# Optimization experiments

Hardware: AMD Instinct MI355X
Metric: run time of the kernel (lower is better)

Reference implementation:

```python
import jax, jax.numpy as jnp
import numpy as np

B, S, D_IN, D, K, KU, L, M, H = 2, 1024, 64, 512, 16, 3, 2, 2, 2048
N_FFT = 2048  # next power of two >= 2*S - 1 (preconvolve padded_sl)
EPS = 1e-5


def setup_inputs() -> dict:
    key = jax.random.key(0)
    ks = jax.random.split(key, 8)
    # Hankel matrix Z[i,j] = 2 / ((i+j)^3 - (i+j)), i,j in 1..S; top-K eigh
    i = np.arange(1, S + 1, dtype=np.float64)
    s = i[:, None] + i[None, :]
    Z = 2.0 / (s ** 3 - s)
    evals, evecs = np.linalg.eigh(Z)
    sigma = jnp.asarray(evals[-K:], jnp.float32)          # (K,)
    phi = jnp.asarray(evecs[:, -K:], jnp.float32)         # (S, K)
    std = D ** -0.5
    return dict(
        inputs=jax.random.normal(ks[0], (B, S, D_IN), jnp.float32),
        sigma=sigma,
        phi=phi,
        in_proj_w=jax.random.normal(ks[1], (M, D, D_IN), jnp.float32) * (D_IN ** -0.5),
        rn_w=jnp.ones((M, L, D), jnp.float32),
        M_u=jax.random.uniform(ks[2], (M, L, KU, D, D), jnp.float32, -std, std),
        M_phi_plus=jax.random.normal(ks[3], (M, L, K, D, D), jnp.float32) * std,
        M_phi_minus=jax.random.normal(ks[4], (M, L, K, D, D), jnp.float32) * std,
        fc1_w=jax.random.normal(ks[5], (M, L, 2 * H, D), jnp.float32) * std,
        fc2_w=jax.random.normal(ks[6], (M, L, D, H), jnp.float32) * (H ** -0.5),
        out_proj_w=jax.random.normal(ks[7], (M, D_IN, D), jnp.float32) * std,
    )


def rmsnorm(x, w):
    return x * jax.lax.rsqrt(jnp.mean(x * x, axis=-1, keepdims=True) + EPS) * w


def compute_spectral(x, sigma, phi, mp, mm):
    # x: (B,S,D); phi: (S,K); mp/mm: (K,D,D)
    sgn = jnp.where(jnp.arange(S) % 2 == 0, 1.0, -1.0).astype(x.dtype)
    u2 = jnp.stack([x, x * sgn[None, :, None]], axis=-1)            # (B,S,D,2)
    U = jnp.fft.rfft(u2, n=N_FFT, axis=1)                           # (B,nf,D,2)
    Vf = jnp.fft.rfft(phi, n=N_FFT, axis=0)                         # (nf,K)
    Uc = jnp.fft.irfft(Vf[None, :, :, None, None] * U[:, :, None, :, :], n=N_FFT, axis=1)[:, :S]  # (B,S,K,D,2)
    Up = Uc[..., 0]
    Um = Uc[..., 1] * sgn[None, :, None, None]
    sig4 = sigma ** 0.25
    return (jnp.einsum('bskd,k,kdo->bso', Up, sig4, mp)
            + jnp.einsum('bskd,k,kdo->bso', Um, sig4, mm))


def compute_ar_u(mu, x):
    # y_t = sum_i x_{t-i} @ M_u[i]; mu: (KU,D,D)
    out = jnp.einsum('bsd,do->bso', x, mu[0])
    for i in range(1, KU):
        xi = jnp.pad(x[:, :S - i], ((0, 0), (i, 0), (0, 0)))
        out = out + jnp.einsum('bsd,do->bso', xi, mu[i])
    return out


def gated_mlp(x, w1, w2):
    y = x @ w1.T
    y, gate = jnp.split(y, 2, axis=-1)
    return (y * jax.nn.silu(gate)) @ w2.T


def reference(inputs, sigma, phi, in_proj_w, rn_w, M_u, M_phi_plus, M_phi_minus, fc1_w, fc2_w, out_proj_w):
    preds = jnp.zeros((B, S, D_IN), inputs.dtype)
    for m in range(M):  # ResidualSTU: sum of per-model predictions
        x = inputs @ in_proj_w[m].T
        for l in range(L):
            z = x
            h = rmsnorm(x, rn_w[m, l])
            spec = compute_spectral(h, sigma, phi, M_phi_plus[m, l], M_phi_minus[m, l])
            y_t = spec + compute_ar_u(M_u[m, l], h)  # use_ar_u=True, use_ar_y=False
            x = x + y_t
            x = x + gated_mlp(x, fc1_w[m, l], fc2_w[m, l])
            x = x + z
        preds = preds + x @ out_proj_w[m].T
    return preds
```

## Files before the change

### kernel.cpp

```cpp
#include <hip/hip_runtime.h>
#include <hip/hip_bf16.h>

typedef _Float16 f16;
typedef _Float16 half8 __attribute__((ext_vector_type(8)));
typedef float f32x4 __attribute__((ext_vector_type(4)));

#define S_LEN 1024
#define DMODEL 512
#define NFFT   2048
#define RPB    2048
#define RTOT   4096
#define CPS    1064
#define NROW   2048
#define NPART  4

__device__ __forceinline__ float2 mkf2(float a, float b) { float2 r; r.x = a; r.y = b; return r; }
__device__ __forceinline__ int zp(int i) { return i + (i >> 5); }
__device__ __forceinline__ float2 cmul(float2 w, float2 b) {
  return mkf2(b.x * w.x - b.y * w.y, b.x * w.y + b.y * w.x);
}
__device__ __forceinline__ float2 f2a(float2 a, float2 b) { return mkf2(a.x + b.x, a.y + b.y); }
__device__ __forceinline__ float2 f2s(float2 a, float2 b) { return mkf2(a.x - b.x, a.y - b.y); }

__device__ __forceinline__ void gl16(const f16* g, f16* l) {
  __builtin_amdgcn_global_load_lds((const __attribute__((address_space(1))) void*)g,
                                   (__attribute__((address_space(3))) void*)l, 16, 0, 0);
}

template<bool INV>
__device__ __forceinline__ void fft2048(float2* z, const float2* __restrict__ tw, int tid) {
  for (int i = tid; i < 2048; i += 256) {
    int j = (int)(__brev((unsigned)i) >> 21);
    if (i < j) { float2 a = z[zp(i)]; z[zp(i)] = z[zp(j)]; z[zp(j)] = a; }
  }
  __syncthreads();
#pragma unroll
  for (int r8 = 0; r8 < 3; ++r8) {
    const int sl = 1 + 3 * r8;
    const int h = 1 << (sl - 1);
    {
      int q = tid;
      int j = q & (h - 1);
      int i0 = ((q >> (sl - 1)) << (sl + 2)) + j;
      float2 a0 = z[zp(i0)],         a1 = z[zp(i0 + h)];
      float2 a2 = z[zp(i0 + 2 * h)], a3 = z[zp(i0 + 3 * h)];
      float2 a4 = z[zp(i0 + 4 * h)], a5 = z[zp(i0 + 5 * h)];
      float2 a6 = z[zp(i0 + 6 * h)], a7 = z[zp(i0 + 7 * h)];
      float2 wA  = tw[j << (11 - sl)];
      float2 wB0 = tw[j << (10 - sl)];
      float2 wB1 = tw[(j + h) << (10 - sl)];
      float2 wC0 = tw[j << (9 - sl)];
      float2 wC1 = tw[(j + h) << (9 - sl)];
      float2 wC2 = tw[(j + 2 * h) << (9 - sl)];
      float2 wC3 = tw[(j + 3 * h) << (9 - sl)];
      if (INV) {
        wA.y = -wA.y; wB0.y = -wB0.y; wB1.y = -wB1.y;
        wC0.y = -wC0.y; wC1.y = -wC1.y; wC2.y = -wC2.y; wC3.y = -wC3.y;
      }
      float2 t;
      t = cmul(wA, a1); float2 b0 = f2a(a0, t), b1 = f2s(a0, t);
      t = cmul(wA, a3); float2 b2 = f2a(a2, t), b3 = f2s(a2, t);
      t = cmul(wA, a5); float2 b4 = f2a(a4, t), b5 = f2s(a4, t);
      t = cmul(wA, a7); float2 b6 = f2a(a6, t), b7 = f2s(a6, t);
      t = cmul(wB0, b2); float2 c0 = f2a(b0, t), c2 = f2s(b0, t);
      t = cmul(wB1, b3); float2 c1 = f2a(b1, t), c3 = f2s(b1, t);
      t = cmul(wB0, b6); float2 c4 = f2a(b4, t), c6 = f2s(b4, t);
      t = cmul(wB1, b7); float2 c5 = f2a(b5, t), c7 = f2s(b5, t);
      t = cmul(wC0, c4); z[zp(i0)]         = f2a(c0, t); z[zp(i0 + 4 * h)] = f2s(c0, t);
      t = cmul(wC1, c5); z[zp(i0 + h)]     = f2a(c1, t); z[zp(i0 + 5 * h)] = f2s(c1, t);
      t = cmul(wC2, c6); z[zp(i0 + 2 * h)] = f2a(c2, t); z[zp(i0 + 6 * h)] = f2s(c2, t);
      t = cmul(wC3, c7); z[zp(i0 + 3 * h)] = f2a(c3, t); z[zp(i0 + 7 * h)] = f2s(c3, t);
    }
    __syncthreads();
  }
  for (int q = tid; q < 512; q += 256) {
    float2 a0 = z[zp(q)], a1 = z[zp(q + 512)], a2 = z[zp(q + 1024)], a3 = z[zp(q + 1536)];
    float2 w1 = tw[q << 1], w2 = tw[q], w3 = tw[q + 512];
    if (INV) { w1.y = -w1.y; w2.y = -w2.y; w3.y = -w3.y; }
    float2 t;
    t = cmul(w1, a1); float2 b0 = f2a(a0, t), b1 = f2s(a0, t);
    t = cmul(w1, a3); float2 b2 = f2a(a2, t), b3 = f2s(a2, t);
    t = cmul(w2, b2); z[zp(q)]        = f2a(b0, t); z[zp(q + 1024)] = f2s(b0, t);
    t = cmul(w3, b3); z[zp(q + 512)]  = f2a(b1, t); z[zp(q + 1536)] = f2s(b1, t);
  }
  __syncthreads();
}

__global__ void k_twiddle(float2* tw) {
  int i = blockIdx.x * 256 + threadIdx.x;
  if (i < 1024) {
    float ang = -6.2831853071795864769f * (float)i / 2048.0f;
    tw[i] = mkf2(cosf(ang), sinf(ang));
  }
}

__global__ void k_fft_phi(const float* __restrict__ phi, float2* __restrict__ Vf,
                          const float2* __restrict__ tw) {
  __shared__ float2 z[2112];
  int tid = threadIdx.x;
  int k0 = blockIdx.x * 2;
  for (int t = tid; t < 1024; t += 256)
    z[zp(t)] = *(const float2*)(phi + (size_t)t * 16 + k0);
  for (int t = 1024 + tid; t < 2048; t += 256) z[zp(t)] = mkf2(0.f, 0.f);
  __syncthreads();
  fft2048<false>(z, tw, tid);
  for (int f = tid; f <= 1024; f += 256) {
    float2 zf = z[zp(f)], zc = z[zp((2048 - f) & 2047)];
    Vf[(size_t)k0 * 1025 + f]       = mkf2(0.5f * (zf.x + zc.x), 0.5f * (zf.y - zc.y));
    Vf[(size_t)(k0 + 1) * 1025 + f] = mkf2(0.5f * (zf.y + zc.y), 0.5f * (zc.x - zf.x));
  }
}

__global__ void k_cpcm(const float2* __restrict__ Vf, const float* __restrict__ sigma,
                       float2* __restrict__ cpcm) {
  int idx = blockIdx.x * 256 + threadIdx.x;
  if (idx >= 32 * CPS) return;
  int kb = idx / CPS, f = idx - kb * CPS;
  int k = kb & 15;
  float s = powf(sigma[k], 0.25f) * (1.0f / 2048.0f);
  float2 v = mkf2(0.f, 0.f);
  if (f == 0) {
    float dc = Vf[(size_t)k * 1025].x;
    float ny = Vf[(size_t)k * 1025 + 1024].x;
    v = (kb < 16) ? mkf2(s * dc, s * ny) : mkf2(s * ny, s * dc);
  } else if (f <= 1023) {
    if (kb < 16) {
      v = Vf[(size_t)k * 1025 + f];
    } else {
      float2 t = Vf[(size_t)k * 1025 + (1024 - f)];
      v = mkf2(t.x, -t.y);
    }
    v.x *= s; v.y *= s;
  }
  cpcm[idx] = v;
}

__global__ __launch_bounds__(256)
void k_fwdcast(const f16* __restrict__ hb2, f16* __restrict__ Xbf,
               const float2* __restrict__ tw, int li,
               const float* __restrict__ Mp, const float* __restrict__ Mm,
               const float* __restrict__ Mu, const float* __restrict__ Fc1,
               const float* __restrict__ Fc2,
               f16* __restrict__ Wsp, f16* __restrict__ Wu,
               f16* __restrict__ Wf1, f16* __restrict__ Wf2) {
  __shared__ __align__(16) char smem[16896];
  int wg = (int)blockIdx.x, tid = threadIdx.x;
  if (wg < 1024) {
    float2* z = (float2*)smem;
    int model = wg >> 9;
    int b = (wg >> 8) & 1;
    int d0 = (wg & 255) * 2;
    const f16* hsrc = hb2 + (size_t)(model * 2 + b) * 1026 * 512;
    f16* xdst = Xbf + (size_t)model * RTOT * 512 + (size_t)b * RPB * 512;
    for (int t = tid; t < 1024; t += 256) {
      union { unsigned v; f16 q[2]; } w;
      w.v = *(const unsigned*)(hsrc + (size_t)(2 + t) * 512 + d0);
      z[zp(t)] = mkf2((float)w.q[0], (float)w.q[1]);
    }
    for (int t = 1024 + tid; t < 2048; t += 256) z[zp(t)] = mkf2(0.f, 0.f);
    __syncthreads();
    fft2048<false>(z, tw, tid);
    for (int f = tid; f <= 1024; f += 256) {
      float2 zf = z[zp(f)], zc = z[zp((2048 - f) & 2047)];
      float x0r = 0.5f * (zf.x + zc.x), x0i = 0.5f * (zf.y - zc.y);
      float x1r = 0.5f * (zf.y + zc.y), x1i = 0.5f * (zc.x - zf.x);
      union { f16 h2[2]; unsigned u; } pr, pi;
      pr.h2[0] = (f16)x0r; pr.h2[1] = (f16)x1r;
      pi.h2[0] = (f16)x0i; pi.h2[1] = (f16)x1i;
      if (f == 0) {
        *(unsigned*)(xdst + d0) = pr.u;
      } else if (f == 1024) {
        *(unsigned*)(xdst + (size_t)512 + d0) = pr.u;
      } else {
        *(unsigned*)(xdst + (size_t)(2 * f) * 512 + d0)     = pr.u;
        *(unsigned*)(xdst + (size_t)(2 * f + 1) * 512 + d0) = pi.u;
      }
    }
    return;
  }
  float* T = (float*)smem;
  int q0all = wg - 1024;
  int model = q0all & 1;
  int blk = q0all >> 1;
  int ml = model * 2 + li;
  const float* mp  = Mp  + (size_t)ml * 16 * 262144;
  const float* mm  = Mm  + (size_t)ml * 16 * 262144;
  const float* mu  = Mu  + (size_t)ml * 3 * 262144;
  const float* fc1 = Fc1 + (size_t)ml * 4096 * 512;
  const float* fc2 = Fc2 + (size_t)ml * 512 * 2048;
  f16* WspM = Wsp + (size_t)model * 16384 * 512;
  f16* WuM  = Wu  + (size_t)model * 512 * 1536;
  f16* Wf1M = Wf1 + (size_t)model * 4096 * 512;
  f16* Wf2M = Wf2 + (size_t)model * 512 * 2048;
  if (blk < 2048) {
    int mat = blk >> 6, tile = blk & 63;
    int d0 = (tile >> 3) * 64, o0 = (tile & 7) * 64;
    const float* src = (mat < 16) ? (mp + (size_t)mat * 262144)
                                  : (mm + (size_t)(mat - 16) * 262144);
    for (int q = tid; q < 4096; q += 256) {
      int i = q >> 6, j = q & 63;
      T[i * 65 + j] = src[(size_t)(d0 + i) * 512 + o0 + j];
    }
    __syncthreads();
    for (int q = tid; q < 4096; q += 256) {
      int i = q >> 6, j = q & 63;
      WspM[(size_t)(mat * 512 + o0 + i) * 512 + d0 + j] = (f16)T[j * 65 + i];
    }
  } else if (blk < 2240) {
    int q1 = blk - 2048;
    int ip = q1 >> 6, tile = q1 & 63;
    int d0 = (tile >> 3) * 64, o0 = (tile & 7) * 64;
    const float* src = mu + (size_t)(2 - ip) * 262144;
    for (int q = tid; q < 4096; q += 256) {
      int i = q >> 6, j = q & 63;
      T[i * 65 + j] = src[(size_t)(d0 + i) * 512 + o0 + j];
    }
    __syncthreads();
    for (int q = tid; q < 4096; q += 256) {
      int i = q >> 6, j = q & 63;
      WuM[(size_t)(o0 + i) * 1536 + ip * 512 + d0 + j] = (f16)T[j * 65 + i];
    }
  } else if (blk < 3264) {
    int q1 = blk - 2240;
    size_t e = ((size_t)q1 * 256 + tid) * 8;
    int jj = (int)(e >> 9), col = (int)(e & 511);
    int srow = (jj & 1) ? (2048 + (jj >> 1)) : (jj >> 1);
    const float4* s = (const float4*)(fc1 + (size_t)srow * 512 + col);
    float4 a = s[0], b = s[1];
    union { f16 h[8]; uint4 u; } pk;
    pk.h[0] = (f16)a.x; pk.h[1] = (f16)a.y; pk.h[2] = (f16)a.z; pk.h[3] = (f16)a.w;
    pk.h[4] = (f16)b.x; pk.h[5] = (f16)b.y; pk.h[6] = (f16)b.z; pk.h[7] = (f16)b.w;
    *(uint4*)(Wf1M + (size_t)jj * 512 + col) = pk.u;
  } else {
    int q1 = blk - 3264;
    size_t e = ((size_t)q1 * 256 + tid) * 8;
    const float4* s = (const float4*)(fc2 + e);
    float4 a = s[0], b = s[1];
    union { f16 h[8]; uint4 u; } pk;
    pk.h[0] = (f16)a.x; pk.h[1] = (f16)a.y; pk.h[2] = (f16)a.z; pk.h[3] = (f16)a.w;
    pk.h[4] = (f16)b.x; pk.h[5] = (f16)b.y; pk.h[6] = (f16)b.z; pk.h[7] = (f16)b.w;
    *(uint4*)(Wf2M + e) = pk.u;
  }
}

__global__ void k_rmsnorm(const f16* __restrict__ x, const float* __restrict__ rn_w, int li,
                          f16* __restrict__ hb2) {
  int tid = threadIdx.x, l = tid & 63, wv = tid >> 6;
  int r = blockIdx.x * 4 + wv;
  int model = r >> 11;
  int rl = r & 2047;
  int b = rl >> 10, t = rl & 1023;
  const float* w = rn_w + (size_t)(model * 2 + li) * 512;
  const f16* xr = x + (size_t)r * 512;
  f16* hr = hb2 + (size_t)((model * 2 + b) * 1026 + 2 + t) * 512;
  float v[8]; float ss = 0.f;
#pragma unroll
  for (int j = 0; j < 8; ++j) { v[j] = (float)xr[j * 64 + l]; ss += v[j] * v[j]; }
#pragma unroll
  for (int o = 32; o; o >>= 1) ss += __shfl_xor(ss, o, 64);
  float rn = rsqrtf(ss * (1.f / 512.f) + 1e-5f);
#pragma unroll
  for (int j = 0; j < 8; ++j) {
    float hv = v[j] * rn * w[j * 64 + l];
    hr[j * 64 + l] = (f16)hv;
  }
}

__global__ void k_fft_inv(const f16* __restrict__ P, f16* __restrict__ spec,
                          const float2* __restrict__ tw) {
  __shared__ float2 z[2112];
  int tid = threadIdx.x;
  int wg = (int)blockIdx.x;
  int model = wg >> 9;
  int b = (wg >> 8) & 1;
  int o0 = (wg & 255) * 2;
  const f16* Pm = P + (size_t)model * 512 * RTOT;
  for (int fp = tid; fp < 512; fp += 256) {
    int f0 = fp * 2;
    size_t base0 = (size_t)o0 * RTOT + (size_t)b * RPB + 2 * f0;
    float s0r[2] = {0.f, 0.f}, s0i[2] = {0.f, 0.f};
    float s1r[2] = {0.f, 0.f}, s1i[2] = {0.f, 0.f};
#pragma unroll
    for (int g = 0; g < NPART; ++g) {
      const f16* Pg = Pm + (size_t)g * (2ull * 512 * RTOT);
      union { uint2 u; f16 h[4]; } ua, uc;
      ua.u = *(const uint2*)(Pg + base0);
      uc.u = *(const uint2*)(Pg + base0 + RTOT);
      s0r[0] += (float)ua.h[0]; s0i[0] += (float)ua.h[1];
      s0r[1] += (float)ua.h[2]; s0i[1] += (float)ua.h[3];
      s1r[0] += (float)uc.h[0]; s1i[0] += (float)uc.h[1];
      s1r[1] += (float)uc.h[2]; s1i[1] += (float)uc.h[3];
    }
    if (fp == 0) {
      z[zp(0)]    = mkf2(s0r[0], s1r[0]);
      z[zp(1024)] = mkf2(s0i[0], s1i[0]);
    } else {
      z[zp(f0)]        = mkf2(s0r[0] - s1i[0], s0i[0] + s1r[0]);
      z[zp(2048 - f0)] = mkf2(s0r[0] + s1i[0], s1r[0] - s0i[0]);
    }
    int f1 = f0 + 1;
    z[zp(f1)]        = mkf2(s0r[1] - s1i[1], s0i[1] + s1r[1]);
    z[zp(2048 - f1)] = mkf2(s0r[1] + s1i[1], s1r[1] - s0i[1]);
  }
  __syncthreads();
  fft2048<true>(z, tw, tid);
  f16* sdst = spec + (size_t)(model * 2048 + b * 1024) * 512;
  for (int t = tid; t < 1024; t += 256) {
    float2 v = z[zp(t)];
    union { f16 h[2]; unsigned u; } pk;
    pk.h[0] = (f16)v.x; pk.h[1] = (f16)v.y;
    *(unsigned*)(sdst + (size_t)t * 512 + o0) = pk.u;
  }
}

__global__ __launch_bounds__(256, 2)
void k_gemm0(const f16* __restrict__ A0, const f16* __restrict__ B00,
             const float* __restrict__ aux0, f16* __restrict__ outP) {
  __shared__ __align__(16) f16 As[128 * 64];
  __shared__ __align__(16) f16 Bs[128 * 64];
  const int tid = threadIdx.x, l = tid & 63, wvi = tid >> 6;
  const int wr = wvi >> 1, wc = wvi & 1;
  int wg = (int)blockIdx.x;
  wg = (wg & 7) * 128 + (wg >> 3);
  const int model = wg >> 9;
  int rem = wg & 511;
  const int bz = rem >> 7; rem &= 127;
  const int by = rem >> 2, bx = rem & 3;
  const int r0 = by * 128, c0 = bx * 128;
  const f16* A  = A0  + (size_t)model * RTOT * 512;
  const f16* B0 = B00 + (size_t)model * 16384 * 512;

  f32x4 acc[4][4];
  f32x4 crun[4][4];
  f32x4 zz = {0.f, 0.f, 0.f, 0.f};
#pragma unroll
  for (int m = 0; m < 4; ++m)
#pragma unroll
    for (int n = 0; n < 4; ++n) { acc[m][n] = zz; crun[m][n] = zz; }

  const int rowl = tid >> 3;
  const int lc8 = ((tid & 7) ^ (rowl & 7)) * 8;
  f16* lA = As + ((tid >> 6) << 9);
  f16* lB = Bs + ((tid >> 6) << 9);
  const int lr = l & 15, kg = l >> 4, sw = l & 7;

  for (int s = 0; s < 64; ++s) {
    __syncthreads();
    {
      const int kA = (s & 7) * 64;
      const int kb = bz * 8 + (s >> 3);
#pragma unroll
      for (int i = 0; i < 4; ++i) {
        gl16(A + (size_t)(r0 + i * 32 + rowl) * 512 + kA + lc8, lA + i * 2048);
        gl16(B0 + (size_t)(kb * 512 + c0 + i * 32 + rowl) * 512 + kA + lc8, lB + i * 2048);
      }
    }
    __syncthreads();
#pragma unroll
    for (int kk = 0; kk < 2; ++kk) {
      half8 af[4], bf[4];
      const int pc8 = (((kk * 4 + kg) ^ sw) << 3);
#pragma unroll
      for (int m = 0; m < 4; ++m)
        af[m] = *(const half8*)(As + (wr * 64 + m * 16 + lr) * 64 + pc8);
#pragma unroll
      for (int n = 0; n < 4; ++n)
        bf[n] = *(const half8*)(Bs + (wc * 64 + n * 16 + lr) * 64 + pc8);
#pragma unroll
      for (int m = 0; m < 4; ++m)
#pragma unroll
        for (int n = 0; n < 4; ++n)
          acc[m][n] = __builtin_amdgcn_mfma_f32_16x16x32_f16(af[m], bf[n], acc[m][n], 0, 0, 0);
    }
    if ((s & 7) == 7) {
      int kb = bz * 8 + (s >> 3);
#pragma unroll
      for (int m = 0; m < 4; ++m) {
        int R = r0 + wr * 64 + m * 16 + (kg << 2);
        int rb = R & (RPB - 1);
        bool dc = (rb == 0);
        float4 cs = *(const float4*)(aux0 + (size_t)kb * (CPS * 2) + (rb >> 1) * 2);
        float t1 = dc ? 0.f : cs.y;
        float t2 = dc ? cs.y : cs.x;
#pragma unroll
        for (int n = 0; n < 4; ++n) {
          f32x4 p = acc[m][n];
          crun[m][n].x += cs.x * p.x - t1 * p.y;
          crun[m][n].y += t2 * p.y + t1 * p.x;
          crun[m][n].z += cs.z * p.z - cs.w * p.w;
          crun[m][n].w += cs.z * p.w + cs.w * p.z;
          acc[m][n] = zz;
        }
      }
    }
  }

  f16* P = outP + (size_t)bz * (2ull * 512 * RTOT) + (size_t)model * 512 * RTOT;
#pragma unroll
  for (int m = 0; m < 4; ++m) {
    int R0 = r0 + wr * 64 + m * 16 + (kg << 2);
#pragma unroll
    for (int n = 0; n < 4; ++n) {
      int o = c0 + wc * 64 + n * 16 + lr;
      union { f16 h[4]; uint2 u; } pk;
      pk.h[0] = (f16)crun[m][n].x; pk.h[1] = (f16)crun[m][n].y;
      pk.h[2] = (f16)crun[m][n].z; pk.h[3] = (f16)crun[m][n].w;
      *(uint2*)(P + (size_t)o * RTOT + R0) = pk.u;
    }
  }
}

template<int MODE, int MR, int NR>
__device__ __forceinline__ void stage(const f16* __restrict__ A, const f16* __restrict__ B0,
                                      int r0, int c0, int tid, int s,
                                      f16* As, f16* Bs) {
  constexpr int LDA = (MODE == 1) ? 1536 : (MODE == 2) ? 512 : 2048;
  const int kA = s * 64;
  const int rowl = tid >> 3;
  const int lc8 = ((tid & 7) ^ (rowl & 7)) * 8;
  f16* lA = As + ((tid >> 6) << 9);
  f16* lB = Bs + ((tid >> 6) << 9);
#pragma unroll
  for (int i = 0; i < MR; ++i) {
    int row = i * 32 + rowl;
    gl16(A + (size_t)(r0 + row) * LDA + kA + lc8, lA + i * 2048);
  }
#pragma unroll
  for (int i = 0; i < NR; ++i) {
    int row = i * 32 + rowl;
    const f16* bs;
    if constexpr (MODE == 1) {
      int ip = s >> 3, d0 = (s & 7) * 64;
      int rr = c0 + row;
      int b = rr >> 10, t = rr & 1023;
      bs = B0 + (size_t)(b * 1026 + t + ip) * 512 + d0 + lc8;
    } else {
      constexpr int LDB = (MODE == 2) ? 512 : 2048;
      bs = B0 + (size_t)(c0 + row) * LDB + s * 64 + lc8;
    }
    gl16(bs, lB + i * 2048);
  }
}

template<int MR, int NR>
__device__ __forceinline__ void mma_step(const f16* As, const f16* Bs, int l, int wr, int wc,
                                         f32x4 acc[MR][NR]) {
  const int lr = l & 15, kg = l >> 4, sw = l & 7;
#pragma unroll
  for (int kk = 0; kk < 2; ++kk) {
    half8 af[MR], bf[NR];
    const int pc8 = (((kk * 4 + kg) ^ sw) << 3);
#pragma unroll
    for (int m = 0; m < MR; ++m)
      af[m] = *(const half8*)(As + (wr * (MR * 16) + m * 16 + lr) * 64 + pc8);
#pragma unroll
    for (int n = 0; n < NR; ++n)
      bf[n] = *(const half8*)(Bs + (wc * (NR * 16) + n * 16 + lr) * 64 + pc8);
#pragma unroll
    for (int m = 0; m < MR; ++m)
#pragma unroll
      for (int n = 0; n < NR; ++n)
        acc[m][n] = __builtin_amdgcn_mfma_f32_16x16x32_f16(af[m], bf[n], acc[m][n], 0, 0, 0);
  }
}

template<int MODE, int MR, int NR>
__global__ __launch_bounds__(256, (MODE == 2) ? 3 : 4)
void k_gemm(const f16* __restrict__ Ain, const f16* __restrict__ Bin,
            const f16* auxAin, const f16* auxBin, f16* __restrict__ outIn) {
  __shared__ __align__(16) f16 As[MR * 32 * 64];
  __shared__ __align__(16) f16 Bs[NR * 32 * 64];
  const int tid = threadIdx.x, l = tid & 63, wvi = tid >> 6;
  const int wr = wvi >> 1, wc = wvi & 1;
  const int bx = blockIdx.x, byi = blockIdx.y;
  constexpr int BYD = (MODE == 2) ? 32 : 8;
  const int model = byi / BYD, by = byi % BYD;
  const int r0 = by * (MR * 32), c0 = bx * (NR * 32);
  constexpr int KS = (MODE == 1) ? 24 : (MODE == 2) ? 8 : 32;
  const size_t actOff = (size_t)model * 2048 * 512;
  const f16* A = Ain + (size_t)model *
      ((MODE == 1) ? 512ull * 1536 : (MODE == 2) ? 4096ull * 512 : 512ull * 2048);
  const f16* B0 = Bin + ((MODE == 1) ? (size_t)model * 2 * 1026 * 512 :
                         (MODE == 2) ? actOff : (size_t)model * 2048 * 2048);
  const f16* auxA = auxAin + actOff;
  const f16* auxB = auxBin + actOff;
  f16* outH = outIn + ((MODE == 2) ? (size_t)model * 2048 * 2048 : actOff);

  f32x4 acc[MR][NR];
  f32x4 zz = {0.f, 0.f, 0.f, 0.f};
#pragma unroll
  for (int m = 0; m < MR; ++m)
#pragma unroll
    for (int n = 0; n < NR; ++n) acc[m][n] = zz;

  for (int s = 0; s < KS; ++s) {
    __syncthreads();
    stage<MODE, MR, NR>(A, B0, r0, c0, tid, s, As, Bs);
    __syncthreads();
    mma_step<MR, NR>(As, Bs, l, wr, wc, acc);
  }

  if constexpr (MODE == 1) {
#pragma unroll
    for (int m = 0; m < MR; ++m) {
      int o0 = r0 + wr * (MR * 16) + m * 16 + ((l >> 4) << 2);
#pragma unroll
      for (int n = 0; n < NR; ++n) {
        int r = c0 + wc * (NR * 16) + n * 16 + (l & 15);
        union { uint2 u; f16 h[4]; } xv, sv;
        xv.u = *(const uint2*)(auxA + (size_t)r * 512 + o0);
        sv.u = *(const uint2*)(auxB + (size_t)r * 512 + o0);
        f32x4 a = acc[m][n];
        union { f16 h[4]; uint2 u; } pk;
        pk.h[0] = (f16)((float)xv.h[0] + (float)sv.h[0] + a.x);
        pk.h[1] = (f16)((float)xv.h[1] + (float)sv.h[1] + a.y);
        pk.h[2] = (f16)((float)xv.h[2] + (float)sv.h[2] + a.z);
        pk.h[3] = (f16)((float)xv.h[3] + (float)sv.h[3] + a.w);
        *(uint2*)(outH + (size_t)r * 512 + o0) = pk.u;
      }
    }
  } else if constexpr (MODE == 2) {
#pragma unroll
    for (int m = 0; m < MR; ++m) {
      int jj0 = r0 + wr * (MR * 16) + m * 16 + ((l >> 4) << 2);
      int h2 = jj0 >> 1;
#pragma unroll
      for (int n = 0; n < NR; ++n) {
        int r = c0 + wc * (NR * 16) + n * 16 + (l & 15);
        f32x4 a = acc[m][n];
        float v0 = a.x * (a.y / (1.f + __expf(-a.y)));
        float v1 = a.z * (a.w / (1.f + __expf(-a.w)));
        union { f16 h[2]; unsigned u; } pk;
        pk.h[0] = (f16)v0; pk.h[1] = (f16)v1;
        *(unsigned*)(outH + (size_t)r * 2048 + h2) = pk.u;
      }
    }
  } else {
#pragma unroll
    for (int m = 0; m < MR; ++m) {
      int o0 = r0 + wr * (MR * 16) + m * 16 + ((l >> 4) << 2);
#pragma unroll
      for (int n = 0; n < NR; ++n) {
        int r = c0 + wc * (NR * 16) + n * 16 + (l & 15);
        union { uint2 u; f16 h[4]; } xv, x1v;
        xv.u  = *(const uint2*)(auxA + (size_t)r * 512 + o0);
        x1v.u = *(const uint2*)(auxB + (size_t)r * 512 + o0);
        f32x4 a = acc[m][n];
        union { f16 h[4]; uint2 u; } pk;
        pk.h[0] = (f16)((float)xv.h[0] + (float)x1v.h[0] + a.x);
        pk.h[1] = (f16)((float)xv.h[1] + (float)x1v.h[1] + a.y);
        pk.h[2] = (f16)((float)xv.h[2] + (float)x1v.h[2] + a.z);
        pk.h[3] = (f16)((float)xv.h[3] + (float)x1v.h[3] + a.w);
        *(uint2*)(outH + (size_t)r * 512 + o0) = pk.u;
      }
    }
  }
}

__global__ void k_inproj(const float* __restrict__ inp, const float* __restrict__ Wall,
                         f16* __restrict__ x) {
  __shared__ float row[64];
  int r = blockIdx.x, tid = threadIdx.x;
  int model = r >> 11, rl = r & 2047;
  const float* W = Wall + (size_t)model * 512 * 64;
  if (tid < 64) row[tid] = inp[(size_t)rl * 64 + tid];
  __syncthreads();
  for (int o = tid; o < 512; o += 256) {
    const float* wr = W + (size_t)o * 64;
    float acc = 0.f;
#pragma unroll 8
    for (int q = 0; q < 64; ++q) acc += row[q] * wr[q];
    x[(size_t)r * 512 + o] = (f16)acc;
  }
}

__global__ void k_outproj(const f16* __restrict__ x, const float* __restrict__ Wall,
                          float* out) {
  __shared__ float row[1024];
  int r = blockIdx.x, tid = threadIdx.x;
  for (int i = tid; i < 1024; i += 256) {
    int mdl = i >> 9, c = i & 511;
    row[i] = (float)x[((size_t)mdl * 2048 + r) * 512 + c];
  }
  __syncthreads();
  int o = tid >> 2, part = tid & 3;
  const float* w0 = Wall + (size_t)o * 512 + part * 128;
  const float* w1 = Wall + 64ull * 512 + (size_t)o * 512 + part * 128;
  const float* r0 = row + part * 128;
  const float* r1 = row + 512 + part * 128;
  float acc = 0.f;
#pragma unroll 16
  for (int q = 0; q < 128; ++q) acc += r0[q] * w0[q] + r1[q] * w1[q];
  acc += __shfl_xor(acc, 1, 64);
  acc += __shfl_xor(acc, 2, 64);
  if (part == 0) out[(size_t)r * 64 + o] = acc;
}

extern "C" void kernel_launch(void* const* d_in, const int* in_sizes, int n_in,
                              void* d_out, int out_size, void* d_ws, size_t ws_size,
                              hipStream_t stream) {
  const float* inputs    = (const float*)d_in[0];
  const float* sigma     = (const float*)d_in[1];
  const float* phi       = (const float*)d_in[2];
  const float* in_proj_w = (const float*)d_in[3];
  const float* rn_w      = (const float*)d_in[4];
  const float* M_u       = (const float*)d_in[5];
  const float* M_phi_p   = (const float*)d_in[6];
  const float* M_phi_m   = (const float*)d_in[7];
  const float* fc1       = (const float*)d_in[8];
  const float* fc2       = (const float*)d_in[9];
  const float* out_proj_w= (const float*)d_in[10];
  float* out = (float*)d_out;

  char* ws = (char*)d_ws;
  size_t off = 0;
  auto alloc = [&](size_t bytes) -> void* {
    void* p = ws + off;
    off += (bytes + 255) & ~(size_t)255;
    return p;
  };
  float2* tw   = (float2*)alloc(1024 * 8);
  float2* Vf   = (float2*)alloc((size_t)16 * 1025 * 8);
  float2* cpcm = (float2*)alloc((size_t)32 * CPS * 8);
  f16*    x    = (f16*)alloc((size_t)2 * NROW * 512 * 2);
  f16*    hb2  = (f16*)alloc((size_t)4 * 1026 * 512 * 2);
  f16*    x1   = (f16*)alloc((size_t)2 * NROW * 512 * 2);
  f16*    spec = (f16*)alloc((size_t)2 * NROW * 512 * 2);
  f16*    Xbf  = (f16*)alloc((size_t)2 * RTOT * 512 * 2);
  f16*    P    = (f16*)alloc((size_t)NPART * 2 * 512 * RTOT * 2);
  f16*    g1   = (f16*)alloc((size_t)2 * NROW * 2048 * 2);
  f16*    Wsp  = (f16*)alloc((size_t)2 * 16384 * 512 * 2);
  f16*    Wu   = (f16*)alloc((size_t)2 * 512 * 1536 * 2);
  f16*    Wf1  = (f16*)alloc((size_t)2 * 4096 * 512 * 2);
  f16*    Wf2  = (f16*)alloc((size_t)2 * 512 * 2048 * 2);
  if (off > ws_size) return;

  for (int k = 0; k < 4; ++k)
    hipMemsetAsync(hb2 + (size_t)k * 1026 * 512, 0, 2 * 512 * sizeof(f16), stream);
  k_twiddle<<<4, 256, 0, stream>>>(tw);
  k_fft_phi<<<8, 256, 0, stream>>>(phi, Vf, tw);
  k_cpcm<<<133, 256, 0, stream>>>(Vf, sigma, cpcm);

  k_inproj<<<4096, 256, 0, stream>>>(inputs, in_proj_w, x);
  for (int li = 0; li < 2; ++li) {
    k_rmsnorm<<<1024, 256, 0, stream>>>(x, rn_w, li, hb2);
    k_fwdcast<<<1024 + 7552, 256, 0, stream>>>(
        hb2, Xbf, tw, li, M_phi_p, M_phi_m, M_u, fc1, fc2, Wsp, Wu, Wf1, Wf2);
    k_gemm0<<<dim3(1024), 256, 0, stream>>>(Xbf, Wsp, (const float*)cpcm, P);
    k_fft_inv<<<1024, 256, 0, stream>>>(P, spec, tw);
    k_gemm<1, 2, 2><<<dim3(32, 16), 256, 0, stream>>>(Wu, hb2, x, spec, x1);
    k_gemm<2, 4, 4><<<dim3(16, 64), 256, 0, stream>>>(Wf1, x1, nullptr, nullptr, g1);
    k_gemm<3, 2, 2><<<dim3(32, 16), 256, 0, stream>>>(Wf2, g1, x, x1, x);
  }
  k_outproj<<<NROW, 256, 0, stream>>>(x, out_proj_w, out);
}
```

Measured before the change: 781.7 us.

## Fuse AR-u GEMM into fwdcast launch, fold spectral add into inverse FFT

Moves the autoregressive M_u GEMM into extra workgroups of the forward-FFT/weight-cast kernel, where it writes x + AR term into a partial buffer. The inverse FFT then adds the spectral result directly, which removes the separate spec buffer and one GEMM launch. The M_u weight casting for both layers moves into the in-projection kernel. The spectral GEMM's K-split is halved (NPART 4→2), so it runs with fewer, longer-running workgroups. This trades launch count and memory traffic for less parallelism in gemm0.

```diff
diff --git a/kernel.cpp b/kernel.cpp
--- a/kernel.cpp
+++ b/kernel.cpp
@@ -12,7 +12,7 @@
 #define RTOT   4096
 #define CPS    1064
 #define NROW   2048
-#define NPART  4
+#define NPART  2
 
 __device__ __forceinline__ float2 mkf2(float a, float b) { float2 r; r.x = a; r.y = b; return r; }
 __device__ __forceinline__ int zp(int i) { return i + (i >> 5); }
@@ -135,14 +135,68 @@
   cpcm[idx] = v;
 }
 
+template<int MODE, int MR, int NR>
+__device__ __forceinline__ void stage(const f16* __restrict__ A, const f16* __restrict__ B0,
+                                      int r0, int c0, int tid, int s,
+                                      f16* As, f16* Bs) {
+  constexpr int LDA = (MODE == 1) ? 1536 : (MODE == 2) ? 512 : 2048;
+  const int kA = s * 64;
+  const int rowl = tid >> 3;
+  const int lc8 = ((tid & 7) ^ (rowl & 7)) * 8;
+  f16* lA = As + ((tid >> 6) << 9);
+  f16* lB = Bs + ((tid >> 6) << 9);
+#pragma unroll
+  for (int i = 0; i < MR; ++i) {
+    int row = i * 32 + rowl;
+    gl16(A + (size_t)(r0 + row) * LDA + kA + lc8, lA + i * 2048);
+  }
+#pragma unroll
+  for (int i = 0; i < NR; ++i) {
+    int row = i * 32 + rowl;
+    const f16* bs;
+    if constexpr (MODE == 1) {
+      int ip = s >> 3, d0 = (s & 7) * 64;
+      int rr = c0 + row;
+      int b = rr >> 10, t = rr & 1023;
+      bs = B0 + (size_t)(b * 1026 + t + ip) * 512 + d0 + lc8;
+    } else {
+      constexpr int LDB = (MODE == 2) ? 512 : 2048;
+      bs = B0 + (size_t)(c0 + row) * LDB + s * 64 + lc8;
+    }
+    gl16(bs, lB + i * 2048);
+  }
+}
+
+template<int MR, int NR>
+__device__ __forceinline__ void mma_step(const f16* As, const f16* Bs, int l, int wr, int wc,
+                                         f32x4 acc[MR][NR]) {
+  const int lr = l & 15, kg = l >> 4, sw = l & 7;
+#pragma unroll
+  for (int kk = 0; kk < 2; ++kk) {
+    half8 af[MR], bf[NR];
+    const int pc8 = (((kk * 4 + kg) ^ sw) << 3);
+#pragma unroll
+    for (int m = 0; m < MR; ++m)
+      af[m] = *(const half8*)(As + (wr * (MR * 16) + m * 16 + lr) * 64 + pc8);
+#pragma unroll
+    for (int n = 0; n < NR; ++n)
+      bf[n] = *(const half8*)(Bs + (wc * (NR * 16) + n * 16 + lr) * 64 + pc8);
+#pragma unroll
+    for (int m = 0; m < MR; ++m)
+#pragma unroll
+      for (int n = 0; n < NR; ++n)
+        acc[m][n] = __builtin_amdgcn_mfma_f32_16x16x32_f16(af[m], bf[n], acc[m][n], 0, 0, 0);
+  }
+}
+
 __global__ __launch_bounds__(256)
 void k_fwdcast(const f16* __restrict__ hb2, f16* __restrict__ Xbf,
                const float2* __restrict__ tw, int li,
                const float* __restrict__ Mp, const float* __restrict__ Mm,
-               const float* __restrict__ Mu, const float* __restrict__ Fc1,
-               const float* __restrict__ Fc2,
-               f16* __restrict__ Wsp, f16* __restrict__ Wu,
-               f16* __restrict__ Wf1, f16* __restrict__ Wf2) {
+               const float* __restrict__ Fc1, const float* __restrict__ Fc2,
+               f16* __restrict__ Wsp, const f16* __restrict__ WuAll,
+               f16* __restrict__ Wf1, f16* __restrict__ Wf2,
+               const f16* __restrict__ x, f16* __restrict__ x1p) {
   __shared__ __align__(16) char smem[16896];
   int wg = (int)blockIdx.x, tid = threadIdx.x;
   if (wg < 1024) {
@@ -178,18 +232,62 @@
     }
     return;
   }
+  if (wg < 1536) {
+    f16* As = (f16*)smem;
+    f16* Bs = (f16*)smem + 4096;
+    int q = wg - 1024;
+    const int bx = q & 31, byi = q >> 5;
+    const int model = byi >> 3, by = byi & 7;
+    const int r0 = by * 64, c0 = bx * 64;
+    const int l = tid & 63, wvi = tid >> 6;
+    const int wr = wvi >> 1, wc = wvi & 1;
+    const f16* A  = WuAll + ((size_t)li * 2 + model) * (512ull * 1536);
+    const f16* B0 = hb2 + (size_t)model * 2 * 1026 * 512;
+    const f16* xM  = x  + (size_t)model * 2048 * 512;
+    f16* x1pM      = x1p + (size_t)model * 2048 * 512;
+
+    f32x4 acc[2][2];
+    f32x4 zz = {0.f, 0.f, 0.f, 0.f};
+#pragma unroll
+    for (int m = 0; m < 2; ++m)
+#pragma unroll
+      for (int n = 0; n < 2; ++n) acc[m][n] = zz;
+
+    for (int s = 0; s < 24; ++s) {
+      __syncthreads();
+      stage<1, 2, 2>(A, B0, r0, c0, tid, s, As, Bs);
+      __syncthreads();
+      mma_step<2, 2>(As, Bs, l, wr, wc, acc);
+    }
+#pragma unroll
+    for (int m = 0; m < 2; ++m) {
+      int o0 = r0 + wr * 32 + m * 16 + ((l >> 4) << 2);
+#pragma unroll
+      for (int n = 0; n < 2; ++n) {
+        int r = c0 + wc * 32 + n * 16 + (l & 15);
+        union { uint2 u; f16 h[4]; } xv;
+        xv.u = *(const uint2*)(xM + (size_t)r * 512 + o0);
+        f32x4 a = acc[m][n];
+        union { f16 h[4]; uint2 u; } pk;
+        pk.h[0] = (f16)((float)xv.h[0] + a.x);
+        pk.h[1] = (f16)((float)xv.h[1] + a.y);
+        pk.h[2] = (f16)((float)xv.h[2] + a.z);
+        pk.h[3] = (f16)((float)xv.h[3] + a.w);
+        *(uint2*)(x1pM + (size_t)r * 512 + o0) = pk.u;
+      }
+    }
+    return;
+  }
   float* T = (float*)smem;
-  int q0all = wg - 1024;
+  int q0all = wg - 1536;
   int model = q0all & 1;
   int blk = q0all >> 1;
   int ml = model * 2 + li;
   const float* mp  = Mp  + (size_t)ml * 16 * 262144;
   const float* mm  = Mm  + (size_t)ml * 16 * 262144;
-  const float* mu  = Mu  + (size_t)ml * 3 * 262144;
   const float* fc1 = Fc1 + (size_t)ml * 4096 * 512;
   const float* fc2 = Fc2 + (size_t)ml * 512 * 2048;
   f16* WspM = Wsp + (size_t)model * 16384 * 512;
-  f16* WuM  = Wu  + (size_t)model * 512 * 1536;
   f16* Wf1M = Wf1 + (size_t)model * 4096 * 512;
   f16* Wf2M = Wf2 + (size_t)model * 512 * 2048;
   if (blk < 2048) {
@@ -206,22 +304,8 @@
       int i = q >> 6, j = q & 63;
       WspM[(size_t)(mat * 512 + o0 + i) * 512 + d0 + j] = (f16)T[j * 65 + i];
     }
-  } else if (blk < 2240) {
+  } else if (blk < 3072) {
     int q1 = blk - 2048;
-    int ip = q1 >> 6, tile = q1 & 63;
-    int d0 = (tile >> 3) * 64, o0 = (tile & 7) * 64;
-    const float* src = mu + (size_t)(2 - ip) * 262144;
-    for (int q = tid; q < 4096; q += 256) {
-      int i = q >> 6, j = q & 63;
-      T[i * 65 + j] = src[(size_t)(d0 + i) * 512 + o0 + j];
-    }
-    __syncthreads();
-    for (int q = tid; q < 4096; q += 256) {
-      int i = q >> 6, j = q & 63;
-      WuM[(size_t)(o0 + i) * 1536 + ip * 512 + d0 + j] = (f16)T[j * 65 + i];
-    }
-  } else if (blk < 3264) {
-    int q1 = blk - 2240;
     size_t e = ((size_t)q1 * 256 + tid) * 8;
     int jj = (int)(e >> 9), col = (int)(e & 511);
     int srow = (jj & 1) ? (2048 + (jj >> 1)) : (jj >> 1);
@@ -232,7 +316,7 @@
     pk.h[4] = (f16)b.x; pk.h[5] = (f16)b.y; pk.h[6] = (f16)b.z; pk.h[7] = (f16)b.w;
     *(uint4*)(Wf1M + (size_t)jj * 512 + col) = pk.u;
   } else {
-    int q1 = blk - 3264;
+    int q1 = blk - 3072;
     size_t e = ((size_t)q1 * 256 + tid) * 8;
     const float4* s = (const float4*)(fc2 + e);
     float4 a = s[0], b = s[1];
@@ -266,8 +350,8 @@
   }
 }
 
-__global__ void k_fft_inv(const f16* __restrict__ P, f16* __restrict__ spec,
-                          const float2* __restrict__ tw) {
+__global__ void k_fft_inv(const f16* __restrict__ P, const f16* __restrict__ x1p,
+                          f16* __restrict__ x1, const float2* __restrict__ tw) {
   __shared__ float2 z[2112];
   int tid = threadIdx.x;
   int wg = (int)blockIdx.x;
@@ -304,12 +388,17 @@
   }
   __syncthreads();
   fft2048<true>(z, tw, tid);
-  f16* sdst = spec + (size_t)(model * 2048 + b * 1024) * 512;
+  size_t rowOff = (size_t)(model * 2048 + b * 1024) * 512;
+  const f16* psrc = x1p + rowOff;
+  f16* pdst = x1 + rowOff;
   for (int t = tid; t < 1024; t += 256) {
     float2 v = z[zp(t)];
+    union { unsigned u; f16 h[2]; } pv;
+    pv.u = *(const unsigned*)(psrc + (size_t)t * 512 + o0);
     union { f16 h[2]; unsigned u; } pk;
-    pk.h[0] = (f16)v.x; pk.h[1] = (f16)v.y;
-    *(unsigned*)(sdst + (size_t)t * 512 + o0) = pk.u;
+    pk.h[0] = (f16)((float)pv.h[0] + v.x);
+    pk.h[1] = (f16)((float)pv.h[1] + v.y);
+    *(unsigned*)(pdst + (size_t)t * 512 + o0) = pk.u;
   }
 }
 
@@ -321,9 +410,9 @@
   const int tid = threadIdx.x, l = tid & 63, wvi = tid >> 6;
   const int wr = wvi >> 1, wc = wvi & 1;
   int wg = (int)blockIdx.x;
-  wg = (wg & 7) * 128 + (wg >> 3);
-  const int model = wg >> 9;
-  int rem = wg & 511;
+  wg = (wg & 7) * 64 + (wg >> 3);
+  const int model = wg >> 8;
+  int rem = wg & 255;
   const int bz = rem >> 7; rem &= 127;
   const int by = rem >> 2, bx = rem & 3;
   const int r0 = by * 128, c0 = bx * 128;
@@ -344,11 +433,11 @@
   f16* lB = Bs + ((tid >> 6) << 9);
   const int lr = l & 15, kg = l >> 4, sw = l & 7;
 
-  for (int s = 0; s < 64; ++s) {
+  for (int s = 0; s < 128; ++s) {
     __syncthreads();
     {
       const int kA = (s & 7) * 64;
-      const int kb = bz * 8 + (s >> 3);
+      const int kb = bz * 16 + (s >> 3);
 #pragma unroll
       for (int i = 0; i < 4; ++i) {
         gl16(A + (size_t)(r0 + i * 32 + rowl) * 512 + kA + lc8, lA + i * 2048);
@@ -373,7 +462,7 @@
           acc[m][n] = __builtin_amdgcn_mfma_f32_16x16x32_f16(af[m], bf[n], acc[m][n], 0, 0, 0);
     }
     if ((s & 7) == 7) {
-      int kb = bz * 8 + (s >> 3);
+      int kb = bz * 16 + (s >> 3);
 #pragma unroll
       for (int m = 0; m < 4; ++m) {
         int R = r0 + wr * 64 + m * 16 + (kg << 2);
@@ -407,60 +496,6 @@
       pk.h[2] = (f16)crun[m][n].z; pk.h[3] = (f16)crun[m][n].w;
       *(uint2*)(P + (size_t)o * RTOT + R0) = pk.u;
     }
-  }
-}
-
-template<int MODE, int MR, int NR>
-__device__ __forceinline__ void stage(const f16* __restrict__ A, const f16* __restrict__ B0,
-                                      int r0, int c0, int tid, int s,
-                                      f16* As, f16* Bs) {
-  constexpr int LDA = (MODE == 1) ? 1536 : (MODE == 2) ? 512 : 2048;
-  const int kA = s * 64;
-  const int rowl = tid >> 3;
-  const int lc8 = ((tid & 7) ^ (rowl & 7)) * 8;
-  f16* lA = As + ((tid >> 6) << 9);
-  f16* lB = Bs + ((tid >> 6) << 9);
-#pragma unroll
-  for (int i = 0; i < MR; ++i) {
-    int row = i * 32 + rowl;
-    gl16(A + (size_t)(r0 + row) * LDA + kA + lc8, lA + i * 2048);
-  }
-#pragma unroll
-  for (int i = 0; i < NR; ++i) {
-    int row = i * 32 + rowl;
-    const f16* bs;
-    if constexpr (MODE == 1) {
-      int ip = s >> 3, d0 = (s & 7) * 64;
-      int rr = c0 + row;
-      int b = rr >> 10, t = rr & 1023;
-      bs = B0 + (size_t)(b * 1026 + t + ip) * 512 + d0 + lc8;
-    } else {
-      constexpr int LDB = (MODE == 2) ? 512 : 2048;
-      bs = B0 + (size_t)(c0 + row) * LDB + s * 64 + lc8;
-    }
-    gl16(bs, lB + i * 2048);
-  }
-}
-
-template<int MR, int NR>
-__device__ __forceinline__ void mma_step(const f16* As, const f16* Bs, int l, int wr, int wc,
-                                         f32x4 acc[MR][NR]) {
-  const int lr = l & 15, kg = l >> 4, sw = l & 7;
-#pragma unroll
-  for (int kk = 0; kk < 2; ++kk) {
-    half8 af[MR], bf[NR];
-    const int pc8 = (((kk * 4 + kg) ^ sw) << 3);
-#pragma unroll
-    for (int m = 0; m < MR; ++m)
-      af[m] = *(const half8*)(As + (wr * (MR * 16) + m * 16 + lr) * 64 + pc8);
-#pragma unroll
-    for (int n = 0; n < NR; ++n)
-      bf[n] = *(const half8*)(Bs + (wc * (NR * 16) + n * 16 + lr) * 64 + pc8);
-#pragma unroll
-    for (int m = 0; m < MR; ++m)
-#pragma unroll
-      for (int n = 0; n < NR; ++n)
-        acc[m][n] = __builtin_amdgcn_mfma_f32_16x16x32_f16(af[m], bf[n], acc[m][n], 0, 0, 0);
   }
 }
 
@@ -476,12 +511,10 @@
   constexpr int BYD = (MODE == 2) ? 32 : 8;
   const int model = byi / BYD, by = byi % BYD;
   const int r0 = by * (MR * 32), c0 = bx * (NR * 32);
-  constexpr int KS = (MODE == 1) ? 24 : (MODE == 2) ? 8 : 32;
+  constexpr int KS = (MODE == 2) ? 8 : 32;
   const size_t actOff = (size_t)model * 2048 * 512;
-  const f16* A = Ain + (size_t)model *
-      ((MODE == 1) ? 512ull * 1536 : (MODE == 2) ? 4096ull * 512 : 512ull * 2048);
-  const f16* B0 = Bin + ((MODE == 1) ? (size_t)model * 2 * 1026 * 512 :
-                         (MODE == 2) ? actOff : (size_t)model * 2048 * 2048);
+  const f16* A = Ain + (size_t)model * ((MODE == 2) ? 4096ull * 512 : 512ull * 2048);
+  const f16* B0 = Bin + ((MODE == 2) ? actOff : (size_t)model * 2048 * 2048);
   const f16* auxA = auxAin + actOff;
   const f16* auxB = auxBin + actOff;
   f16* outH = outIn + ((MODE == 2) ? (size_t)model * 2048 * 2048 : actOff);
@@ -500,26 +533,7 @@
     mma_step<MR, NR>(As, Bs, l, wr, wc, acc);
   }
 
-  if constexpr (MODE == 1) {
-#pragma unroll
-    for (int m = 0; m < MR; ++m) {
-      int o0 = r0 + wr * (MR * 16) + m * 16 + ((l >> 4) << 2);
-#pragma unroll
-      for (int n = 0; n < NR; ++n) {
-        int r = c0 + wc * (NR * 16) + n * 16 + (l & 15);
-        union { uint2 u; f16 h[4]; } xv, sv;
-        xv.u = *(const uint2*)(auxA + (size_t)r * 512 + o0);
-        sv.u = *(const uint2*)(auxB + (size_t)r * 512 + o0);
-        f32x4 a = acc[m][n];
-        union { f16 h[4]; uint2 u; } pk;
-        pk.h[0] = (f16)((float)xv.h[0] + (float)sv.h[0] + a.x);
-        pk.h[1] = (f16)((float)xv.h[1] + (float)sv.h[1] + a.y);
-        pk.h[2] = (f16)((float)xv.h[2] + (float)sv.h[2] + a.z);
-        pk.h[3] = (f16)((float)xv.h[3] + (float)sv.h[3] + a.w);
-        *(uint2*)(outH + (size_t)r * 512 + o0) = pk.u;
-      }
-    }
-  } else if constexpr (MODE == 2) {
+  if constexpr (MODE == 2) {
 #pragma unroll
     for (int m = 0; m < MR; ++m) {
       int jj0 = r0 + wr * (MR * 16) + m * 16 + ((l >> 4) << 2);
@@ -557,20 +571,44 @@
   }
 }
 
-__global__ void k_inproj(const float* __restrict__ inp, const float* __restrict__ Wall,
-                         f16* __restrict__ x) {
-  __shared__ float row[64];
-  int r = blockIdx.x, tid = threadIdx.x;
-  int model = r >> 11, rl = r & 2047;
-  const float* W = Wall + (size_t)model * 512 * 64;
-  if (tid < 64) row[tid] = inp[(size_t)rl * 64 + tid];
+__global__ __launch_bounds__(256)
+void k_inproj(const float* __restrict__ inp, const float* __restrict__ Wall,
+              const float* __restrict__ Mu, f16* __restrict__ x, f16* __restrict__ WuAll) {
+  __shared__ __align__(16) char smem[16900];
+  int wg = (int)blockIdx.x, tid = threadIdx.x;
+  if (wg < 4096) {
+    float* row = (float*)smem;
+    int r = wg;
+    int model = r >> 11, rl = r & 2047;
+    const float* W = Wall + (size_t)model * 512 * 64;
+    if (tid < 64) row[tid] = inp[(size_t)rl * 64 + tid];
+    __syncthreads();
+    for (int o = tid; o < 512; o += 256) {
+      const float* wr = W + (size_t)o * 64;
+      float acc = 0.f;
+#pragma unroll 8
+      for (int q = 0; q < 64; ++q) acc += row[q] * wr[q];
+      x[(size_t)r * 512 + o] = (f16)acc;
+    }
+    return;
+  }
+  float* T = (float*)smem;
+  int q = wg - 4096;
+  int lm = q & 3;
+  int model = lm & 1, li = lm >> 1;
+  int blk = q >> 2;
+  int ip = blk >> 6, tile = blk & 63;
+  int d0 = (tile >> 3) * 64, o0 = (tile & 7) * 64;
+  const float* src = Mu + ((size_t)(model * 2 + li) * 3 + (2 - ip)) * 262144;
+  f16* dst = WuAll + ((size_t)li * 2 + model) * (512ull * 1536);
+  for (int p = tid; p < 4096; p += 256) {
+    int i = p >> 6, j = p & 63;
+    T[i * 65 + j] = src[(size_t)(d0 + i) * 512 + o0 + j];
+  }
   __syncthreads();
-  for (int o = tid; o < 512; o += 256) {
-    const float* wr = W + (size_t)o * 64;
-    float acc = 0.f;
-#pragma unroll 8
-    for (int q = 0; q < 64; ++q) acc += row[q] * wr[q];
-    x[(size_t)r * 512 + o] = (f16)acc;
+  for (int p = tid; p < 4096; p += 256) {
+    int i = p >> 6, j = p & 63;
+    dst[(size_t)(o0 + i) * 1536 + ip * 512 + d0 + j] = (f16)T[j * 65 + i];
   }
 }
 
@@ -624,13 +662,13 @@
   float2* cpcm = (float2*)alloc((size_t)32 * CPS * 8);
   f16*    x    = (f16*)alloc((size_t)2 * NROW * 512 * 2);
   f16*    hb2  = (f16*)alloc((size_t)4 * 1026 * 512 * 2);
+  f16*    x1p  = (f16*)alloc((size_t)2 * NROW * 512 * 2);
   f16*    x1   = (f16*)alloc((size_t)2 * NROW * 512 * 2);
-  f16*    spec = (f16*)alloc((size_t)2 * NROW * 512 * 2);
   f16*    Xbf  = (f16*)alloc((size_t)2 * RTOT * 512 * 2);
   f16*    P    = (f16*)alloc((size_t)NPART * 2 * 512 * RTOT * 2);
   f16*    g1   = (f16*)alloc((size_t)2 * NROW * 2048 * 2);
   f16*    Wsp  = (f16*)alloc((size_t)2 * 16384 * 512 * 2);
-  f16*    Wu   = (f16*)alloc((size_t)2 * 512 * 1536 * 2);
+  f16*    WuA  = (f16*)alloc((size_t)4 * 512 * 1536 * 2);
   f16*    Wf1  = (f16*)alloc((size_t)2 * 4096 * 512 * 2);
   f16*    Wf2  = (f16*)alloc((size_t)2 * 512 * 2048 * 2);
   if (off > ws_size) return;
@@ -641,14 +679,13 @@
   k_fft_phi<<<8, 256, 0, stream>>>(phi, Vf, tw);
   k_cpcm<<<133, 256, 0, stream>>>(Vf, sigma, cpcm);
 
-  k_inproj<<<4096, 256, 0, stream>>>(inputs, in_proj_w, x);
+  k_inproj<<<4096 + 768, 256, 0, stream>>>(inputs, in_proj_w, M_u, x, WuA);
   for (int li = 0; li < 2; ++li) {
     k_rmsnorm<<<1024, 256, 0, stream>>>(x, rn_w, li, hb2);
-    k_fwdcast<<<1024 + 7552, 256, 0, stream>>>(
-        hb2, Xbf, tw, li, M_phi_p, M_phi_m, M_u, fc1, fc2, Wsp, Wu, Wf1, Wf2);
-    k_gemm0<<<dim3(1024), 256, 0, stream>>>(Xbf, Wsp, (const float*)cpcm, P);
-    k_fft_inv<<<1024, 256, 0, stream>>>(P, spec, tw);
-    k_gemm<1, 2, 2><<<dim3(32, 16), 256, 0, stream>>>(Wu, hb2, x, spec, x1);
+    k_fwdcast<<<1024 + 512 + 7168, 256, 0, stream>>>(
+        hb2, Xbf, tw, li, M_phi_p, M_phi_m, fc1, fc2, Wsp, WuA, Wf1, Wf2, x, x1p);
+    k_gemm0<<<dim3(512), 256, 0, stream>>>(Xbf, Wsp, (const float*)cpcm, P);
+    k_fft_inv<<<1024, 256, 0, stream>>>(P, x1p, x1, tw);
     k_gemm<2, 4, 4><<<dim3(16, 64), 256, 0, stream>>>(Wf1, x1, nullptr, nullptr, g1);
     k_gemm<3, 2, 2><<<dim3(32, 16), 256, 0, stream>>>(Wf2, g1, x, x1, x);
   }
```

Result: faster. 749.1 us (-4.2%).
